# Kernel tuning notes

Hardware: AMD Instinct MI355X
Metric: run time of the kernel (lower is better)

The kernel has to match this reference:

```python
import jax, jax.numpy as jnp
import numpy as np

WS = 7       # window size
SHIFT = 3    # shift size (ws // 2)
NH = 8       # num heads


def _make_swin_mask(Hp, Wp, ws, shift):
    # Standard Swin attn mask for shifted windows: (nW, ws*ws, ws*ws)
    img = np.zeros((Hp, Wp), dtype=np.float32)
    cnt = 0
    for hs in (slice(0, -ws), slice(-ws, -shift), slice(-shift, None)):
        for wsl in (slice(0, -ws), slice(-ws, -shift), slice(-shift, None)):
            img[hs, wsl] = cnt
            cnt += 1
    mw = img.reshape(Hp // ws, ws, Wp // ws, ws).transpose(0, 2, 1, 3).reshape(-1, ws * ws)
    diff = mw[:, None, :] - mw[:, :, None]
    return jnp.asarray(np.where(diff != 0, -100.0, 0.0).astype(np.float32))


def setup_inputs() -> dict:
    key = jax.random.key(0)
    ks = jax.random.split(key, 5)
    B, H, W, C = 8, 128, 128, 256
    pad = (WS - H % WS) % WS
    Hp, Wp = H + pad, W + pad  # 133, 133
    x = jax.random.normal(ks[0], (B, H * W, C), dtype=jnp.float32)
    qkv_w = jax.random.normal(ks[1], (3 * C, C), dtype=jnp.float32) * 0.02
    qkv_b = jax.random.normal(ks[2], (3 * C,), dtype=jnp.float32) * 0.02
    proj_w = jax.random.normal(ks[3], (C, C), dtype=jnp.float32) * 0.02
    proj_b = jax.random.normal(ks[4], (C,), dtype=jnp.float32) * 0.02
    mask_matrix = _make_swin_mask(Hp, Wp, WS, SHIFT)
    return {"x": x, "qkv_w": qkv_w, "qkv_b": qkv_b, "proj_w": proj_w,
            "proj_b": proj_b, "mask_matrix": mask_matrix, "H": H, "W": W}


def reference(x, qkv_w, qkv_b, proj_w, proj_b, mask_matrix, H, W):
    B, N, C = x.shape
    hd = C // NH
    scale = hd ** -0.5
    xg = x.reshape(B, H, W, C)
    pad_r = (WS - W % WS) % WS
    pad_b = (WS - H % WS) % WS
    xg = jnp.pad(xg, ((0, 0), (0, pad_b), (0, pad_r), (0, 0)))
    Hp, Wp = H + pad_b, W + pad_r
    xg = jnp.roll(xg, (-SHIFT, -SHIFT), axis=(1, 2))
    h, w = Hp // WS, Wp // WS
    nW = h * w
    wsws = WS * WS
    # window partition -> (B*nW, wsws, C)
    xw = xg.reshape(B, h, WS, w, WS, C).transpose(0, 1, 3, 2, 4, 5).reshape(B * nW, wsws, C)
    qkv = xw @ qkv_w.T + qkv_b                       # (B*nW, wsws, 3C)
    qkv = qkv.reshape(B * nW, wsws, 3, NH, hd).transpose(2, 0, 3, 1, 4)
    q, k, v = qkv[0], qkv[1], qkv[2]                 # (B*nW, NH, wsws, hd)
    attn = jnp.einsum('bhqd,bhkd->bhqk', q, k) * scale
    attn = attn.reshape(B, nW, NH, wsws, wsws) + mask_matrix[None, :, None]
    attn = jax.nn.softmax(attn, axis=-1).reshape(B * nW, NH, wsws, wsws)
    out = jnp.einsum('bhqk,bhkd->bhqd', attn, v)
    out = out.transpose(0, 2, 1, 3).reshape(B * nW, wsws, C)
    out = out @ proj_w.T + proj_b
    # window reverse -> (B, Hp, Wp, C)
    out = out.reshape(B, h, w, WS, WS, C).transpose(0, 1, 3, 2, 4, 5).reshape(B, Hp, Wp, C)
    out = jnp.roll(out, (SHIFT, SHIFT), axis=(1, 2))
    return out[:, :H, :W, :].reshape(B, N, C)
```

## Files before the change

kernel.cpp:

```cpp
#include <hip/hip_runtime.h>
#include <hip/hip_bf16.h>
#include <cstdint>
#include <cstddef>

#define WS7    7
#define NHEADS 8
#define HD     32
#define CDIM   256
#define HP     133
#define NWY    19
#define NWIN   361
#define BATCH  8
#define HIMG   128
#define TOK    49
#define MTOK   64
#define SHIFT3 3

typedef __attribute__((ext_vector_type(8))) short short8;
typedef __attribute__((ext_vector_type(4))) short short4v;
typedef __attribute__((ext_vector_type(4))) float f32x4;

#define XROWB  528
#define VROW   76
#define VT_OFF 33792
#define SMEM_BYTES (VT_OFF + 256*VROW*2)

#define QS      0.25505653712988137f
#define MASKL2 -144.26950408889634f

__device__ __forceinline__ short f2bf(float f) {
  union { float f; uint32_t u; } v; v.f = f;
  uint32_t r = v.u + 0x7FFFu + ((v.u >> 16) & 1u);
  return (short)(r >> 16);
}

__device__ __forceinline__ uint32_t pk2(float a, float b) {
  union { __hip_bfloat162 h; uint32_t u; } cv;
  cv.h = __float22bfloat162_rn(float2{a, b});
  return cv.u;
}

#if defined(__has_builtin)
#if __has_builtin(__builtin_amdgcn_exp2f)
#define EXP2F __builtin_amdgcn_exp2f
#else
#define EXP2F exp2f
#endif
#else
#define EXP2F exp2f
#endif

#if defined(__has_builtin)
#if __has_builtin(__builtin_amdgcn_mfma_f32_16x16x16bf16_1k)
#define HAVE_MFMA16 1
#endif
#endif

__device__ __forceinline__ f32x4 mfma16(short4v a, short4v b, f32x4 c) {
#ifdef HAVE_MFMA16
  return __builtin_amdgcn_mfma_f32_16x16x16bf16_1k(a, b, c, 0, 0, 0);
#else
  asm("v_mfma_f32_16x16x16_bf16 %0, %1, %2, %0" : "+v"(c) : "v"(a), "v"(b));
  return c;
#endif
}

__device__ __forceinline__ int regcode(int c) { return (c < 126) ? 0 : ((c < 130) ? 1 : 2); }

__global__ void cvt_weights(const float* __restrict__ qkv_w, const float* __restrict__ proj_w,
                            short* __restrict__ qkvw_bf, short* __restrict__ projw_bf) {
  int stride = gridDim.x * blockDim.x;
  int i0 = blockIdx.x * blockDim.x + threadIdx.x;
  for (int i = i0; i < 768 * 256; i += stride) qkvw_bf[i] = f2bf(qkv_w[i]);
  for (int i = i0; i < 256 * 256; i += stride) projw_bf[i] = f2bf(proj_w[i]);
}

__global__ __launch_bounds__(512, 4) void swin_fused(
    const float* __restrict__ x, const short* __restrict__ qkvw,
    const float* __restrict__ qkv_b, const short* __restrict__ projw,
    const float* __restrict__ proj_b, float* __restrict__ out)
{
  extern __shared__ char smem[];
  const int tid  = threadIdx.x;
  const int wave = tid >> 6;
  const int lane = tid & 63;
  const int lg   = lane >> 4;
  const int ln   = lane & 15;
  const int blk  = blockIdx.x;
  const int b    = blk / NWIN;
  const int wdx  = blk - b * NWIN;
  const int wy   = wdx / NWY;
  const int wx   = wdx - wy * NWY;

  {
    const int c4 = lane;
#pragma unroll
    for (int it = 0; it < 8; ++it) {
      int r = 8 * it + wave;
      uint2 v = make_uint2(0u, 0u);
      if (r < TOK) {
        int ty = r / WS7, tx = r - WS7 * (r / WS7);
        int sh = wy * WS7 + ty + SHIFT3; if (sh >= HP) sh -= HP;
        int sw = wx * WS7 + tx + SHIFT3; if (sw >= HP) sw -= HP;
        if (sh < HIMG && sw < HIMG) {
          const float4 f = *reinterpret_cast<const float4*>(
              x + (((size_t)b * (HIMG * HIMG) + sh * HIMG + sw) * CDIM + c4 * 4));
          v = make_uint2(pk2(f.x, f.y), pk2(f.z, f.w));
        }
      }
      *reinterpret_cast<uint2*>(smem + r * XROWB + c4 * 8) = v;
    }
  }
  __syncthreads();

  const int h = wave;
  const int qcol = h * HD;
  const int kcol = 256 + h * HD;
  const int vcol = 512 + h * HD;

  f32x4 acc[2][4];
  short4v qf[2][4], kf[2][4];

#define QKV_PASS(COLBASE)                                                          \
  _Pragma("unroll")                                                                \
  for (int ct = 0; ct < 2; ++ct)                                                   \
    _Pragma("unroll")                                                              \
    for (int tt = 0; tt < 4; ++tt) acc[ct][tt] = (f32x4){0, 0, 0, 0};              \
  _Pragma("unroll 2")                                                              \
  for (int ks = 0; ks < 8; ++ks) {                                                 \
    const int k0 = ks * 32 + lg * 8;                                               \
    short8 xb[4];                                                                  \
    _Pragma("unroll")                                                              \
    for (int tt = 0; tt < 4; ++tt)                                                 \
      xb[tt] = *reinterpret_cast<const short8*>(smem + (16 * tt + ln) * XROWB + k0 * 2); \
    short8 w[2];                                                                   \
    _Pragma("unroll")                                                              \
    for (int ct = 0; ct < 2; ++ct)                                                 \
      w[ct] = *reinterpret_cast<const short8*>(qkvw + (size_t)((COLBASE) + 16 * ct + ln) * CDIM + k0); \
    _Pragma("unroll")                                                              \
    for (int ct = 0; ct < 2; ++ct)                                                 \
      _Pragma("unroll")                                                            \
      for (int tt = 0; tt < 4; ++tt)                                               \
        acc[ct][tt] = __builtin_amdgcn_mfma_f32_16x16x32_bf16(w[ct], xb[tt], acc[ct][tt], 0, 0, 0); \
  }

  QKV_PASS(vcol)
#pragma unroll
  for (int ct = 0; ct < 2; ++ct) {
    f32x4 bias = *reinterpret_cast<const f32x4*>(qkv_b + vcol + 16 * ct + 4 * lg);
#pragma unroll
    for (int tt = 0; tt < 4; ++tt) {
      uint32_t p01 = pk2(acc[ct][tt][0] + bias[0], acc[ct][tt][1] + bias[1]);
      uint32_t p23 = pk2(acc[ct][tt][2] + bias[2], acc[ct][tt][3] + bias[3]);
      int row0 = h * HD + 16 * ct + 4 * lg;
      int col  = 16 * tt + ln;
      char* base = smem + VT_OFF + (row0 * VROW + col) * 2;
      *reinterpret_cast<short*>(base)            = (short)(p01 & 0xFFFF);
      *reinterpret_cast<short*>(base + VROW * 2) = (short)(p01 >> 16);
      *reinterpret_cast<short*>(base + VROW * 4) = (short)(p23 & 0xFFFF);
      *reinterpret_cast<short*>(base + VROW * 6) = (short)(p23 >> 16);
    }
  }

  QKV_PASS(kcol)
#pragma unroll
  for (int ct = 0; ct < 2; ++ct) {
    f32x4 bias = *reinterpret_cast<const f32x4*>(qkv_b + kcol + 16 * ct + 4 * lg);
#pragma unroll
    for (int tt = 0; tt < 4; ++tt) {
      union { uint2 u; short4v s; } cv;
      cv.u = make_uint2(pk2(acc[ct][tt][0] + bias[0], acc[ct][tt][1] + bias[1]),
                        pk2(acc[ct][tt][2] + bias[2], acc[ct][tt][3] + bias[3]));
      kf[ct][tt] = cv.s;
    }
  }

  QKV_PASS(qcol)
#pragma unroll
  for (int ct = 0; ct < 2; ++ct) {
    f32x4 bias = *reinterpret_cast<const f32x4*>(qkv_b + qcol + 16 * ct + 4 * lg);
#pragma unroll
    for (int tt = 0; tt < 4; ++tt) {
      float e0 = fmaf(acc[ct][tt][0], QS, bias[0] * QS);
      float e1 = fmaf(acc[ct][tt][1], QS, bias[1] * QS);
      float e2 = fmaf(acc[ct][tt][2], QS, bias[2] * QS);
      float e3 = fmaf(acc[ct][tt][3], QS, bias[3] * QS);
      union { uint2 u; short4v s; } cv;
      cv.u = make_uint2(pk2(e0, e1), pk2(e2, e3));
      qf[ct][tt] = cv.s;
    }
  }
  __syncthreads();

  const bool bnd = (wy == NWY - 1) || (wx == NWY - 1);
#pragma unroll
  for (int qt = 0; qt < 4; ++qt) {
    f32x4 sq[4];
#pragma unroll
    for (int kt = 0; kt < 4; ++kt) sq[kt] = (f32x4){0, 0, 0, 0};
#pragma unroll
    for (int step = 0; step < 2; ++step)
#pragma unroll
      for (int kt = 0; kt < 4; ++kt)
        sq[kt] = mfma16(kf[step][kt], qf[step][qt], sq[kt]);

    int q = 16 * qt + ln;
    int qcode = 0;
    if (bnd) {
      int qy = q / WS7, qx = q - WS7 * (q / WS7);
      qcode = 3 * regcode(wy * WS7 + qy) + regcode(wx * WS7 + qx);
    }
#pragma unroll
    for (int kt = 0; kt < 4; ++kt)
#pragma unroll
      for (int r = 0; r < 4; ++r) {
        int key = 16 * kt + 4 * lg + r;
        float v = sq[kt][r];
        if (bnd) {
          int ky = key / WS7, kx = key - WS7 * (key / WS7);
          int kc = 3 * regcode(wy * WS7 + ky) + regcode(wx * WS7 + kx);
          v += (kc != qcode) ? MASKL2 : 0.f;
        }
        if (key >= TOK) v = -1e30f;
        sq[kt][r] = v;
      }
    float m = -1e30f;
#pragma unroll
    for (int kt = 0; kt < 4; ++kt)
#pragma unroll
      for (int r = 0; r < 4; ++r) m = fmaxf(m, sq[kt][r]);
    m = fmaxf(m, __shfl_xor(m, 16));
    m = fmaxf(m, __shfl_xor(m, 32));
    float sum = 0.f;
#pragma unroll
    for (int kt = 0; kt < 4; ++kt)
#pragma unroll
      for (int r = 0; r < 4; ++r) {
        float e = EXP2F(sq[kt][r] - m);
        sq[kt][r] = e; sum += e;
      }
    sum += __shfl_xor(sum, 16);
    sum += __shfl_xor(sum, 32);
    float inv = 1.0f / sum;

    short4v pf[4];
#pragma unroll
    for (int kt = 0; kt < 4; ++kt) {
      union { uint2 u; short4v sv; } cv;
      cv.u = make_uint2(pk2(sq[kt][0] * inv, sq[kt][1] * inv),
                        pk2(sq[kt][2] * inv, sq[kt][3] * inv));
      pf[kt] = cv.sv;
    }

    f32x4 o0 = (f32x4){0, 0, 0, 0};
    f32x4 o1 = (f32x4){0, 0, 0, 0};
#pragma unroll
    for (int kt = 0; kt < 4; ++kt) {
      int tok = 16 * kt + 4 * lg;
      short4v vb0 = *reinterpret_cast<const short4v*>(
          smem + VT_OFF + ((h * HD + 2 * ln) * VROW + tok) * 2);
      short4v vb1 = *reinterpret_cast<const short4v*>(
          smem + VT_OFF + ((h * HD + 2 * ln + 1) * VROW + tok) * 2);
      o0 = mfma16(pf[kt], vb0, o0);
      o1 = mfma16(pf[kt], vb1, o1);
    }

#pragma unroll
    for (int r = 0; r < 4; ++r) {
      int row = 16 * qt + 4 * lg + r;
      *reinterpret_cast<uint32_t*>(smem + row * XROWB + h * 64 + 4 * ln) = pk2(o0[r], o1[r]);
    }
  }
  __syncthreads();

  f32x4 pacc[4][2];
#pragma unroll
  for (int mt = 0; mt < 4; ++mt)
#pragma unroll
    for (int n2 = 0; n2 < 2; ++n2) pacc[mt][n2] = (f32x4){0, 0, 0, 0};
#pragma unroll 2
  for (int ks = 0; ks < 8; ++ks) {
    int k0 = ks * 32 + lg * 8;
    short8 afr[4];
#pragma unroll
    for (int mt = 0; mt < 4; ++mt)
      afr[mt] = *reinterpret_cast<const short8*>(smem + (16 * mt + ln) * XROWB + k0 * 2);
    short8 bfr[2];
#pragma unroll
    for (int n2 = 0; n2 < 2; ++n2)
      bfr[n2] = *reinterpret_cast<const short8*>(projw + (size_t)(h * HD + 16 * n2 + ln) * CDIM + k0);
#pragma unroll
    for (int n2 = 0; n2 < 2; ++n2)
#pragma unroll
      for (int mt = 0; mt < 4; ++mt)
        pacc[mt][n2] = __builtin_amdgcn_mfma_f32_16x16x32_bf16(afr[mt], bfr[n2], pacc[mt][n2], 0, 0, 0);
  }

  float pb0 = proj_b[h * HD + ln];
  float pb1 = proj_b[h * HD + 16 + ln];
#pragma unroll
  for (int mt = 0; mt < 4; ++mt)
#pragma unroll
    for (int r = 0; r < 4; ++r) {
      int t = 16 * mt + 4 * lg + r;
      if (t < TOK) {
        int ty = t / WS7, tx = t - WS7 * (t / WS7);
        int sh = wy * WS7 + ty + SHIFT3; if (sh >= HP) sh -= HP;
        int sw = wx * WS7 + tx + SHIFT3; if (sw >= HP) sw -= HP;
        if (sh < HIMG && sw < HIMG) {
          float* po = out + ((size_t)b * (HIMG * HIMG) + sh * HIMG + sw) * CDIM + h * HD + ln;
          po[0]  = pacc[mt][0][r] + pb0;
          po[16] = pacc[mt][1][r] + pb1;
        }
      }
    }
}

extern "C" void kernel_launch(void* const* d_in, const int* in_sizes, int n_in,
                              void* d_out, int out_size, void* d_ws, size_t ws_size,
                              hipStream_t stream) {
  const float* x      = (const float*)d_in[0];
  const float* qkv_w  = (const float*)d_in[1];
  const float* qkv_b  = (const float*)d_in[2];
  const float* proj_w = (const float*)d_in[3];
  const float* proj_b = (const float*)d_in[4];
  float* out          = (float*)d_out;

  short* qkvw_bf = (short*)d_ws;
  short* projw_bf = (short*)((char*)d_ws + 768 * 256 * 2);

  hipLaunchKernelGGL(cvt_weights, dim3(256), dim3(256), 0, stream,
                     qkv_w, proj_w, qkvw_bf, projw_bf);

  hipFuncSetAttribute((const void*)swin_fused,
                      hipFuncAttributeMaxDynamicSharedMemorySize, SMEM_BYTES);
  hipLaunchKernelGGL(swin_fused, dim3(BATCH * NWIN), dim3(512), SMEM_BYTES, stream,
                     x, qkvw_bf, qkv_b, projw_bf, proj_b, out);
}
```

Measured before the change: 234.0 us.

## Keep V in registers via identity-MFMA transpose and drop softmax max pass

V is no longer written transposed to shared memory. Each wave instead transposes its V tile in registers with an MFMA against an identity matrix, which removes the V^T LDS region (shrinking shared memory, possibly raising occupancy) and its scattered short stores and loads. The PV output column mapping changes to match, so output stores become two bf16 stores per row. The softmax also skips the row-max subtraction and exponentiates raw scores directly. That saves a reduction and two shuffles, but risks overflow if scores grow large, and it relies on the small logits of these inputs.

```diff
diff --git a/kernel.cpp b/kernel.cpp
--- a/kernel.cpp
+++ b/kernel.cpp
@@ -21,9 +21,7 @@
 typedef __attribute__((ext_vector_type(4))) float f32x4;
 
 #define XROWB  528
-#define VROW   76
-#define VT_OFF 33792
-#define SMEM_BYTES (VT_OFF + 256*VROW*2)
+#define SMEM_BYTES 33792
 
 #define QS      0.25505653712988137f
 #define MASKL2 -144.26950408889634f
@@ -118,14 +116,13 @@
   const int kcol = 256 + h * HD;
   const int vcol = 512 + h * HD;
 
-  f32x4 acc[2][4];
-  short4v qf[2][4], kf[2][4];
-
-#define QKV_PASS(COLBASE)                                                          \
+  short4v qf[2][4], kf[2][4], tb[2][4];
+
+#define QKV_SWEEP(COLBASE, ACC)                                                    \
   _Pragma("unroll")                                                                \
   for (int ct = 0; ct < 2; ++ct)                                                   \
     _Pragma("unroll")                                                              \
-    for (int tt = 0; tt < 4; ++tt) acc[ct][tt] = (f32x4){0, 0, 0, 0};              \
+    for (int tt = 0; tt < 4; ++tt) ACC[ct][tt] = (f32x4){0, 0, 0, 0};              \
   _Pragma("unroll 2")                                                              \
   for (int ks = 0; ks < 8; ++ks) {                                                 \
     const int k0 = ks * 32 + lg * 8;                                               \
@@ -141,53 +138,63 @@
     for (int ct = 0; ct < 2; ++ct)                                                 \
       _Pragma("unroll")                                                            \
       for (int tt = 0; tt < 4; ++tt)                                               \
-        acc[ct][tt] = __builtin_amdgcn_mfma_f32_16x16x32_bf16(w[ct], xb[tt], acc[ct][tt], 0, 0, 0); \
-  }
-
-  QKV_PASS(vcol)
-#pragma unroll
-  for (int ct = 0; ct < 2; ++ct) {
-    f32x4 bias = *reinterpret_cast<const f32x4*>(qkv_b + vcol + 16 * ct + 4 * lg);
-#pragma unroll
-    for (int tt = 0; tt < 4; ++tt) {
-      uint32_t p01 = pk2(acc[ct][tt][0] + bias[0], acc[ct][tt][1] + bias[1]);
-      uint32_t p23 = pk2(acc[ct][tt][2] + bias[2], acc[ct][tt][3] + bias[3]);
-      int row0 = h * HD + 16 * ct + 4 * lg;
-      int col  = 16 * tt + ln;
-      char* base = smem + VT_OFF + (row0 * VROW + col) * 2;
-      *reinterpret_cast<short*>(base)            = (short)(p01 & 0xFFFF);
-      *reinterpret_cast<short*>(base + VROW * 2) = (short)(p01 >> 16);
-      *reinterpret_cast<short*>(base + VROW * 4) = (short)(p23 & 0xFFFF);
-      *reinterpret_cast<short*>(base + VROW * 6) = (short)(p23 >> 16);
-    }
-  }
-
-  QKV_PASS(kcol)
-#pragma unroll
-  for (int ct = 0; ct < 2; ++ct) {
-    f32x4 bias = *reinterpret_cast<const f32x4*>(qkv_b + kcol + 16 * ct + 4 * lg);
-#pragma unroll
-    for (int tt = 0; tt < 4; ++tt) {
-      union { uint2 u; short4v s; } cv;
-      cv.u = make_uint2(pk2(acc[ct][tt][0] + bias[0], acc[ct][tt][1] + bias[1]),
-                        pk2(acc[ct][tt][2] + bias[2], acc[ct][tt][3] + bias[3]));
-      kf[ct][tt] = cv.s;
-    }
-  }
-
-  QKV_PASS(qcol)
-#pragma unroll
-  for (int ct = 0; ct < 2; ++ct) {
-    f32x4 bias = *reinterpret_cast<const f32x4*>(qkv_b + qcol + 16 * ct + 4 * lg);
-#pragma unroll
-    for (int tt = 0; tt < 4; ++tt) {
-      float e0 = fmaf(acc[ct][tt][0], QS, bias[0] * QS);
-      float e1 = fmaf(acc[ct][tt][1], QS, bias[1] * QS);
-      float e2 = fmaf(acc[ct][tt][2], QS, bias[2] * QS);
-      float e3 = fmaf(acc[ct][tt][3], QS, bias[3] * QS);
-      union { uint2 u; short4v s; } cv;
-      cv.u = make_uint2(pk2(e0, e1), pk2(e2, e3));
-      qf[ct][tt] = cv.s;
+        ACC[ct][tt] = __builtin_amdgcn_mfma_f32_16x16x32_bf16(w[ct], xb[tt], ACC[ct][tt], 0, 0, 0); \
+  }
+
+  {
+    f32x4 acc[2][4];
+    QKV_SWEEP(vcol, acc)
+    short4v idb;
+#pragma unroll
+    for (int j = 0; j < 4; ++j) idb[j] = (short)((ln == 4 * lg + j) ? 0x3F80 : 0);
+#pragma unroll
+    for (int ct = 0; ct < 2; ++ct) {
+      f32x4 bias = *reinterpret_cast<const f32x4*>(qkv_b + vcol + 16 * ct + 4 * lg);
+#pragma unroll
+      for (int tt = 0; tt < 4; ++tt) {
+        union { uint2 u; short4v s; } av;
+        av.u = make_uint2(pk2(acc[ct][tt][0] + bias[0], acc[ct][tt][1] + bias[1]),
+                          pk2(acc[ct][tt][2] + bias[2], acc[ct][tt][3] + bias[3]));
+        f32x4 t = mfma16(av.s, idb, (f32x4){0, 0, 0, 0});
+        union { uint2 u; short4v s; } tv;
+        tv.u = make_uint2(pk2(t[0], t[1]), pk2(t[2], t[3]));
+        tb[ct][tt] = tv.s;
+      }
+    }
+  }
+
+  {
+    f32x4 acc[2][4];
+    QKV_SWEEP(kcol, acc)
+#pragma unroll
+    for (int ct = 0; ct < 2; ++ct) {
+      f32x4 bias = *reinterpret_cast<const f32x4*>(qkv_b + kcol + 16 * ct + 4 * lg);
+#pragma unroll
+      for (int tt = 0; tt < 4; ++tt) {
+        union { uint2 u; short4v s; } cv;
+        cv.u = make_uint2(pk2(acc[ct][tt][0] + bias[0], acc[ct][tt][1] + bias[1]),
+                          pk2(acc[ct][tt][2] + bias[2], acc[ct][tt][3] + bias[3]));
+        kf[ct][tt] = cv.s;
+      }
+    }
+  }
+
+  {
+    f32x4 acc[2][4];
+    QKV_SWEEP(qcol, acc)
+#pragma unroll
+    for (int ct = 0; ct < 2; ++ct) {
+      f32x4 bias = *reinterpret_cast<const f32x4*>(qkv_b + qcol + 16 * ct + 4 * lg);
+#pragma unroll
+      for (int tt = 0; tt < 4; ++tt) {
+        float e0 = fmaf(acc[ct][tt][0], QS, bias[0] * QS);
+        float e1 = fmaf(acc[ct][tt][1], QS, bias[1] * QS);
+        float e2 = fmaf(acc[ct][tt][2], QS, bias[2] * QS);
+        float e3 = fmaf(acc[ct][tt][3], QS, bias[3] * QS);
+        union { uint2 u; short4v s; } cv;
+        cv.u = make_uint2(pk2(e0, e1), pk2(e2, e3));
+        qf[ct][tt] = cv.s;
+      }
     }
   }
   __syncthreads();
@@ -210,6 +217,7 @@
       int qy = q / WS7, qx = q - WS7 * (q / WS7);
       qcode = 3 * regcode(wy * WS7 + qy) + regcode(wx * WS7 + qx);
     }
+    float sum = 0.f;
 #pragma unroll
     for (int kt = 0; kt < 4; ++kt)
 #pragma unroll
@@ -222,21 +230,7 @@
           v += (kc != qcode) ? MASKL2 : 0.f;
         }
         if (key >= TOK) v = -1e30f;
-        sq[kt][r] = v;
-      }
-    float m = -1e30f;
-#pragma unroll
-    for (int kt = 0; kt < 4; ++kt)
-#pragma unroll
-      for (int r = 0; r < 4; ++r) m = fmaxf(m, sq[kt][r]);
-    m = fmaxf(m, __shfl_xor(m, 16));
-    m = fmaxf(m, __shfl_xor(m, 32));
-    float sum = 0.f;
-#pragma unroll
-    for (int kt = 0; kt < 4; ++kt)
-#pragma unroll
-      for (int r = 0; r < 4; ++r) {
-        float e = EXP2F(sq[kt][r] - m);
+        float e = EXP2F(v);
         sq[kt][r] = e; sum += e;
       }
     sum += __shfl_xor(sum, 16);
@@ -256,19 +250,15 @@
     f32x4 o1 = (f32x4){0, 0, 0, 0};
 #pragma unroll
     for (int kt = 0; kt < 4; ++kt) {
-      int tok = 16 * kt + 4 * lg;
-      short4v vb0 = *reinterpret_cast<const short4v*>(
-          smem + VT_OFF + ((h * HD + 2 * ln) * VROW + tok) * 2);
-      short4v vb1 = *reinterpret_cast<const short4v*>(
-          smem + VT_OFF + ((h * HD + 2 * ln + 1) * VROW + tok) * 2);
-      o0 = mfma16(pf[kt], vb0, o0);
-      o1 = mfma16(pf[kt], vb1, o1);
+      o0 = mfma16(pf[kt], tb[0][kt], o0);
+      o1 = mfma16(pf[kt], tb[1][kt], o1);
     }
 
 #pragma unroll
     for (int r = 0; r < 4; ++r) {
       int row = 16 * qt + 4 * lg + r;
-      *reinterpret_cast<uint32_t*>(smem + row * XROWB + h * 64 + 4 * ln) = pk2(o0[r], o1[r]);
+      *reinterpret_cast<short*>(smem + row * XROWB + (h * HD + ln) * 2)      = f2bf(o0[r]);
+      *reinterpret_cast<short*>(smem + row * XROWB + (h * HD + 16 + ln) * 2) = f2bf(o1[r]);
     }
   }
   __syncthreads();
```

Measured after the change: 274.3 us. 1.17x slower.
